# Kernel tuning notes

Measured on AMD Instinct MI355X. Metric: run time of the kernel, lower is better.

## Reference

```python
import jax, jax.numpy as jnp
import numpy as np
from jax import lax


def _conv_block(x, w, b):
    # conv5x5 stride1 VALID + bias, ReLU, maxpool 2x2 stride 2 (NCHW)
    y = lax.conv_general_dilated(x, w, (1, 1), 'VALID',
                                 dimension_numbers=('NCHW', 'OIHW', 'NCHW'))
    y = jax.nn.relu(y + b[None, :, None, None])
    return lax.reduce_window(y, -np.inf, lax.max, (1, 1, 2, 2), (1, 1, 2, 2), 'VALID')


def _attention(feat, g, w, b):
    # feat: [B,C,H,W]; g: [B,512]; Linear(512 -> C)
    q = g @ w.T + b  # [B,C]
    Bn, C, H, W = feat.shape
    f = feat.reshape(Bn, C, H * W)
    # compat_scores[b,n] = sum_c f[b,c,n] * q[b,c] ; softmax over spatial dim
    a = jax.nn.softmax(jnp.einsum('bcn,bc->bn', f, q), axis=1)
    # weighted sum over spatial locations -> [B,C]
    return jnp.einsum('bcn,bn->bc', f, a)


def setup_inputs() -> dict:
    key = jax.random.key(0)
    ks = jax.random.split(key, 12)
    s = 0.02
    f32 = jnp.float32
    return {
        'x': jax.random.normal(ks[0], (16, 1, 220, 220), f32),
        'w1': jax.random.normal(ks[1], (64, 1, 5, 5), f32) * s,
        'b1': jnp.zeros((64,), f32),
        'w2': jax.random.normal(ks[2], (128, 64, 5, 5), f32) * s,
        'b2': jnp.zeros((128,), f32),
        'w3': jax.random.normal(ks[3], (256, 128, 5, 5), f32) * s,
        'b3': jnp.zeros((256,), f32),
        'fcw': jax.random.normal(ks[4], (512, 256 * 24 * 24), f32) * 0.002,
        'fcb': jnp.zeros((512,), f32),
        'aw1': jax.random.normal(ks[5], (64, 512), f32) * s,
        'ab1': jnp.zeros((64,), f32),
        'aw2': jax.random.normal(ks[6], (128, 512), f32) * s,
        'ab2': jnp.zeros((128,), f32),
        'aw3': jax.random.normal(ks[7], (256, 512), f32) * s,
        'ab3': jnp.zeros((256,), f32),
    }


def reference(x, w1, b1, w2, b2, w3, b3, fcw, fcb, aw1, ab1, aw2, ab2, aw3, ab3):
    o1 = _conv_block(x, w1, b1)    # [B,64,108,108]
    o2 = _conv_block(o1, w2, b2)   # [B,128,52,52]
    o3 = _conv_block(o2, w3, b3)   # [B,256,24,24]
    # dropout layers are identity at inference
    flat = o3.reshape(o3.shape[0], -1)          # [B, 256*24*24]
    g = flat @ fcw.T + fcb                       # [B, 512]
    att1 = _attention(o1, g, aw1, ab1)           # [B, 64]
    att2 = _attention(o2, g, aw2, ab2)           # [B, 128]
    att3 = _attention(o3, g, aw3, ab3)           # [B, 256]
    return jnp.concatenate([att1, att2, att3], axis=1)  # [B, 448]
```

## Files before the change

### kernel.cpp

```cpp
#include <hip/hip_runtime.h>
#include <cstdint>

typedef __attribute__((ext_vector_type(8))) short short8;
typedef __attribute__((ext_vector_type(4))) float f32x4;

__device__ __forceinline__ ushort f2bf(float f) {
  union { float f; uint32_t u; } v; v.f = f;
  uint32_t u = v.u;
  return (ushort)((u + 0x7fffu + ((u >> 16) & 1u)) >> 16);
}
__device__ __forceinline__ float bf2f(ushort h) {
  union { uint32_t u; float f; } v; v.u = ((uint32_t)h) << 16;
  return v.f;
}

__global__ __launch_bounds__(256) void prelude_k(
    const float* __restrict__ x, const float* __restrict__ w1, const float* __restrict__ b1,
    const float* __restrict__ w2, const float* __restrict__ w3,
    ushort* __restrict__ o1, ushort* __restrict__ w2t, ushort* __restrict__ w3t,
    float* __restrict__ g, float* __restrict__ out) {
  __shared__ ushort sb[28 * 29];
  const int tid = threadIdx.x;
  const int bx = blockIdx.x;
  if (bx >= 1296) {
    if (bx < 4496) {
      int idx = (bx - 1296) * 256 + tid;
      if (idx < 204800) {
        int j = idx & 7, lane = (idx >> 3) & 63, ks = (idx >> 9) & 1,
            fo = (idx >> 10) & 7, kpos = idx >> 13;
        int oc = fo * 16 + (lane & 15);
        int ic = ks * 32 + (lane >> 4) * 8 + j;
        w2t[idx] = f2bf(w2[((size_t)oc * 64 + ic) * 25 + kpos]);
      }
      {
        int j = idx & 7, lane = (idx >> 3) & 63, ks = (idx >> 9) & 3,
            fo = (idx >> 11) & 15, kpos = idx >> 15;
        int oc = fo * 16 + (lane & 15);
        int ic = ks * 32 + (lane >> 4) * 8 + j;
        w3t[idx] = f2bf(w3[((size_t)oc * 128 + ic) * 25 + kpos]);
      }
    } else {
      for (int i = tid; i < 8192; i += 256) g[i] = 0.f;
      for (int i = tid; i < 7168; i += 256) out[i] = 0.f;
    }
    return;
  }
  const int b = bx / 81, rem = bx % 81, ty = rem / 9, tx = rem % 9;
  for (int i = tid; i < 784; i += 256) {
    int iy = i / 28, ix = i % 28;
    sb[iy * 29 + ix] = f2bf(x[((size_t)b * 220 + ty * 24 + iy) * 220 + tx * 24 + ix]);
  }
  __syncthreads();
  const int lane = tid & 63, wid = tid >> 6;
  const int m16 = lane & 15, qd = lane >> 4;
  short8 bfr[4];
#pragma unroll
  for (int n = 0; n < 4; n++) {
    union { ushort u[8]; short8 v; } t;
#pragma unroll
    for (int j = 0; j < 8; j++) {
      int k = qd * 8 + j;
      int kc = k < 25 ? k : 0;
      ushort val = f2bf(w1[(n * 16 + m16) * 25 + kc]);
      t.u[j] = (k < 25) ? val : (ushort)0;
    }
    bfr[n] = t.v;
  }
  int offs[8];
#pragma unroll
  for (int j = 0; j < 8; j++) {
    int k = qd * 8 + j;
    int kc = k < 25 ? k : 24;
    offs[j] = (kc / 5) * 29 + (kc % 5);
  }
  float bias[4];
#pragma unroll
  for (int n = 0; n < 4; n++) bias[n] = b1[n * 16 + m16];
  for (int gg = 0; gg < 9; gg++) {
    int gr = wid * 9 + gg;
    int wglob = gr * 4 + (m16 >> 2);
    int wy = wglob / 12, wx = wglob % 12;
    int py = wy * 2 + ((m16 >> 1) & 1), px = wx * 2 + (m16 & 1);
    int base = py * 29 + px;
    union { ushort u[8]; short8 v; } a;
#pragma unroll
    for (int j = 0; j < 8; j++) a.u[j] = sb[base + offs[j]];
    int wgd = gr * 4 + qd;
    int gy = ty * 12 + wgd / 12, gx = tx * 12 + wgd % 12;
    size_t oidx = (((size_t)b * 108 + gy) * 108 + gx) * 64;
#pragma unroll
    for (int n = 0; n < 4; n++) {
      f32x4 d = (f32x4){0.f, 0.f, 0.f, 0.f};
      d = __builtin_amdgcn_mfma_f32_16x16x32_bf16(a.v, bfr[n], d, 0, 0, 0);
      float mx = fmaxf(fmaxf(d[0], d[1]), fmaxf(d[2], d[3]));
      o1[oidx + n * 16 + m16] = f2bf(fmaxf(mx + bias[n], 0.f));
    }
  }
}

template <int IC, int ICP, int OCT, int WOC, int INW, int POOLW>
__global__ __launch_bounds__(256, 3) void conv_mfma(const ushort* __restrict__ in,
                                                    const ushort* __restrict__ wt,
                                                    const float* __restrict__ bias,
                                                    ushort* __restrict__ out) {
  constexpr int NB = 4 / WOC;
  constexpr int NPIX = 144;
  constexpr int PSTRIDE = OCT + 8;
  constexpr int LDSA = NB * NPIX * ICP;
  constexpr int LDSP = NB * 64 * PSTRIDE;
  constexpr int LDSN = (LDSA > LDSP) ? LDSA : LDSP;
  constexpr int NKS = IC / 32;
  constexpr int NFRAG = OCT / 16;
  __shared__ ushort sm[LDSN];
  const int tid = threadIdx.x;
  const int wid = tid >> 6, lane = tid & 63;
  const int m16 = lane & 15, qd = lane >> 4;
  const int bh = wid / WOC, og = wid % WOC;
  const int b0 = blockIdx.z * NB;
  const int ty = blockIdx.y, tx = blockIdx.x;
  {
    constexpr int C8 = IC / 8;
    for (int i = tid; i < NB * NPIX * C8; i += 256) {
      int bb = i / (NPIX * C8), rem = i % (NPIX * C8);
      int px = rem / C8, c8 = rem % C8;
      int gy = ty * 8 + px / 12, gx = tx * 8 + px % 12;
      uint4 v = *(const uint4*)(in + (((size_t)(b0 + bb) * INW + gy) * INW + gx) * IC + c8 * 8);
      *(uint4*)&sm[(bb * NPIX + px) * ICP + c8 * 8] = v;
    }
  }
  __syncthreads();
  f32x4 acc[4][4];
#pragma unroll
  for (int i = 0; i < 4; i++)
#pragma unroll
    for (int j = 0; j < 4; j++) acc[i][j] = (f32x4){0.f, 0.f, 0.f, 0.f};
  int aoff[4];
#pragma unroll
  for (int ms = 0; ms < 4; ms++) {
    int p = ms * 16 + m16;
    aoff[ms] = (bh * NPIX + (p >> 3) * 12 + (p & 7)) * ICP + qd * 8;
  }
  const int fo0 = og * 4;
  for (int ky = 0; ky < 5; ky++) {
#pragma unroll
    for (int kx = 0; kx < 5; kx++) {
      const int koff = (ky * 12 + kx) * ICP;
      const ushort* wkp = wt + (((size_t)(ky * 5 + kx) * NFRAG + fo0) * NKS) * 512 + lane * 8;
#pragma unroll
      for (int ks = 0; ks < NKS; ks++) {
        short8 afr[4], bfr[4];
#pragma unroll
        for (int ms = 0; ms < 4; ms++)
          afr[ms] = *(const short8*)&sm[aoff[ms] + koff + ks * 32];
#pragma unroll
        for (int ns = 0; ns < 4; ns++)
          bfr[ns] = *(const short8*)(wkp + (ns * NKS + ks) * 512);
#pragma unroll
        for (int ms = 0; ms < 4; ms++)
#pragma unroll
          for (int ns = 0; ns < 4; ns++)
            acc[ms][ns] = __builtin_amdgcn_mfma_f32_16x16x32_bf16(afr[ms], bfr[ns], acc[ms][ns], 0, 0, 0);
      }
    }
  }
  __syncthreads();
#pragma unroll
  for (int ms = 0; ms < 4; ms++)
#pragma unroll
    for (int ns = 0; ns < 4; ns++) {
      int ocl = og * 64 + ns * 16 + m16;
      float bv = bias[ocl];
#pragma unroll
      for (int r = 0; r < 4; r++) {
        int p = ms * 16 + qd * 4 + r;
        sm[(bh * 64 + p) * PSTRIDE + ocl] = f2bf(fmaxf(acc[ms][ns][r] + bv, 0.f));
      }
    }
  __syncthreads();
  constexpr int OC2 = OCT / 2;
  const int oc2 = tid % OC2, pst = tid / OC2;
  for (int pp = pst; pp < NB * 16; pp += 256 / OC2) {
    int bb = pp >> 4, pl = pp & 15;
    int ppy = pl >> 2, ppx = pl & 3;
    int p00 = (ppy * 2) * 8 + ppx * 2;
    int oc = oc2 * 2;
    int base = bb * 64 * PSTRIDE;
    uint32_t v0 = *(const uint32_t*)&sm[base + p00 * PSTRIDE + oc];
    uint32_t v1 = *(const uint32_t*)&sm[base + (p00 + 1) * PSTRIDE + oc];
    uint32_t v2 = *(const uint32_t*)&sm[base + (p00 + 8) * PSTRIDE + oc];
    uint32_t v3 = *(const uint32_t*)&sm[base + (p00 + 9) * PSTRIDE + oc];
    float a0 = fmaxf(fmaxf(bf2f(v0 & 0xffff), bf2f(v1 & 0xffff)),
                     fmaxf(bf2f(v2 & 0xffff), bf2f(v3 & 0xffff)));
    float a1 = fmaxf(fmaxf(bf2f(v0 >> 16), bf2f(v1 >> 16)),
                     fmaxf(bf2f(v2 >> 16), bf2f(v3 >> 16)));
    uint32_t packed = ((uint32_t)f2bf(a1) << 16) | (uint32_t)f2bf(a0);
    int gy = ty * 4 + ppy, gx = tx * 4 + ppx;
    *(uint32_t*)&out[(((size_t)(b0 + bb) * POOLW + gy) * POOLW + gx) * OCT + oc] = packed;
  }
}

__global__ void transpose_o3(const ushort* __restrict__ o3, ushort* __restrict__ flatT) {
  __shared__ ushort t[32][33];
  const int b = blockIdx.z;
  const int n0 = blockIdx.x * 32, c0 = blockIdx.y * 32;
  const int tid = threadIdx.x;
  {
    int cl = tid & 31, r = tid >> 5;
    for (int i = 0; i < 4; i++) {
      int nl = r + i * 8;
      t[nl][cl] = o3[((size_t)b * 576 + n0 + nl) * 256 + c0 + cl];
    }
  }
  __syncthreads();
  {
    int nl = tid & 31, r = tid >> 5;
    for (int i = 0; i < 4; i++) {
      int cl = r + i * 8;
      flatT[(size_t)b * 147456 + (c0 + cl) * 576 + n0 + nl] = t[nl][cl];
    }
  }
}

__global__ void fc_mfma(const ushort* __restrict__ flatT, const float* __restrict__ fcw,
                        float* __restrict__ g) {
  const int tid = threadIdx.x;
  const int wid = tid >> 6, lane = tid & 63;
  const int m16 = lane & 15, qd = lane >> 4;
  const int jt = blockIdx.y * 256 + wid * 64;
  const int K0 = blockIdx.x * 384;
  f32x4 acc[4];
#pragma unroll
  for (int f = 0; f < 4; f++) acc[f] = (f32x4){0.f, 0.f, 0.f, 0.f};
  const ushort* ap = flatT + (size_t)m16 * 147456 + K0 + qd * 8;
  const float* bp = fcw + (size_t)(jt + m16) * 147456 + K0 + qd * 8;
#pragma unroll 2
  for (int ks = 0; ks < 12; ks++) {
    short8 a = *(const short8*)(ap + ks * 32);
#pragma unroll
    for (int f = 0; f < 4; f++) {
      const float* bpf = bp + (size_t)f * 16 * 147456 + ks * 32;
      float4 b0 = *(const float4*)bpf;
      float4 b1 = *(const float4*)(bpf + 4);
      short8 bb;
      bb[0] = (short)f2bf(b0.x); bb[1] = (short)f2bf(b0.y);
      bb[2] = (short)f2bf(b0.z); bb[3] = (short)f2bf(b0.w);
      bb[4] = (short)f2bf(b1.x); bb[5] = (short)f2bf(b1.y);
      bb[6] = (short)f2bf(b1.z); bb[7] = (short)f2bf(b1.w);
      acc[f] = __builtin_amdgcn_mfma_f32_16x16x32_bf16(a, bb, acc[f], 0, 0, 0);
    }
  }
  const int brow = qd * 4;
#pragma unroll
  for (int f = 0; f < 4; f++)
#pragma unroll
    for (int r = 0; r < 4; r++)
      atomicAdd(&g[(brow + r) * 512 + jt + f * 16 + m16], acc[f][r]);
}

__global__ __launch_bounds__(256) void qcalc(const float* __restrict__ g,
                                             const float* __restrict__ fcb,
                                             const float* __restrict__ aw1, const float* __restrict__ ab1,
                                             const float* __restrict__ aw2, const float* __restrict__ ab2,
                                             const float* __restrict__ aw3, const float* __restrict__ ab3,
                                             float* __restrict__ q) {
  const int b = blockIdx.x, tid = threadIdx.x;
  const int cpart = blockIdx.y;
  __shared__ float gs[512];
  for (int i = tid; i < 512; i += 256) gs[i] = g[b * 512 + i] + fcb[i];
  __syncthreads();
  for (int c = cpart * 224 + tid; c < cpart * 224 + 224; c += 256) {
    const float* ar;
    float acc;
    if (c < 64)       { ar = aw1 + (size_t)c * 512;         acc = ab1[c]; }
    else if (c < 192) { ar = aw2 + (size_t)(c - 64) * 512;  acc = ab2[c - 64]; }
    else              { ar = aw3 + (size_t)(c - 192) * 512; acc = ab3[c - 192]; }
#pragma unroll 4
    for (int j = 0; j < 512; j += 4) {
      float4 a4 = *(const float4*)(ar + j);
      acc += a4.x * gs[j] + a4.y * gs[j + 1] + a4.z * gs[j + 2] + a4.w * gs[j + 3];
    }
    q[b * 448 + c] = acc;
  }
}

template <int C, int COFF>
__device__ __forceinline__ void score_head(const ushort* __restrict__ f,
                                           const float* __restrict__ q,
                                           float* __restrict__ s, int N, int nblk, int b,
                                           float* sq) {
  const int tid = threadIdx.x;
  if (tid < C) sq[tid] = q[b * 448 + COFF + tid];
  __syncthreads();
  int n = nblk * 256 + tid;
  if (n >= N) return;
  const ushort* fr = f + ((size_t)b * N + n) * C;
  float acc = 0.f;
#pragma unroll
  for (int c0 = 0; c0 < C; c0 += 8) {
    uint4 v = *(const uint4*)&fr[c0];
    uint32_t arr[4] = {v.x, v.y, v.z, v.w};
#pragma unroll
    for (int k = 0; k < 4; k++) {
      acc += bf2f(arr[k] & 0xffff) * sq[c0 + 2 * k];
      acc += bf2f(arr[k] >> 16) * sq[c0 + 2 * k + 1];
    }
  }
  s[(size_t)b * N + n] = acc;
}

__global__ void scores_all(const ushort* __restrict__ o1, const ushort* __restrict__ o2,
                           const ushort* __restrict__ o3, const float* __restrict__ q,
                           float* __restrict__ s1, float* __restrict__ s2,
                           float* __restrict__ s3) {
  __shared__ float sq[256];
  const int bx = blockIdx.x, b = blockIdx.y;
  if (bx < 46)      score_head<64, 0>(o1, q, s1, 11664, bx, b, sq);
  else if (bx < 57) score_head<128, 64>(o2, q, s2, 2704, bx - 46, b, sq);
  else              score_head<256, 192>(o3, q, s3, 576, bx - 57, b, sq);
}

__global__ void stats_all(const float* __restrict__ s1, const float* __restrict__ s2,
                          const float* __restrict__ s3, float* __restrict__ st) {
  const int b = blockIdx.x, head = blockIdx.y, tid = threadIdx.x;
  const float* s; int N; float* stp;
  if (head == 0)      { s = s1; N = 11664; stp = st; }
  else if (head == 1) { s = s2; N = 2704;  stp = st + 32; }
  else                { s = s3; N = 576;   stp = st + 64; }
  const float* sb = s + (size_t)b * N;
  __shared__ float red[4];
  float m = -1e30f;
  for (int i = tid; i < N; i += 256) m = fmaxf(m, sb[i]);
  for (int o = 32; o; o >>= 1) m = fmaxf(m, __shfl_xor(m, o));
  if ((tid & 63) == 0) red[tid >> 6] = m;
  __syncthreads();
  m = fmaxf(fmaxf(red[0], red[1]), fmaxf(red[2], red[3]));
  __syncthreads();
  float l = 0.f;
  for (int i = tid; i < N; i += 256) l += __expf(sb[i] - m);
  for (int o = 32; o; o >>= 1) l += __shfl_xor(l, o);
  if ((tid & 63) == 0) red[tid >> 6] = l;
  __syncthreads();
  if (tid == 0) { stp[b * 2] = m; stp[b * 2 + 1] = red[0] + red[1] + red[2] + red[3]; }
}

template <int C, int COFF, int CHUNK>
__device__ __forceinline__ void wsum_head(const ushort* __restrict__ f,
                                          const float* __restrict__ s,
                                          const float* __restrict__ st,
                                          float* __restrict__ out, int N, int nblk, int b,
                                          float* ws, float* os) {
  const int tid = threadIdx.x;
  const float m = st[b * 2], rl = 1.f / st[b * 2 + 1];
  const float* sb = s + (size_t)b * N;
  const ushort* fb = f + (size_t)b * N * C;
  const int n0 = nblk * CHUNK;
  int n1 = n0 + CHUNK; if (n1 > N) n1 = N;
  const int L = n1 - n0;
  for (int i = tid; i < L; i += 256) ws[i] = __expf(sb[n0 + i] - m);
  for (int i = tid; i < C; i += 256) os[i] = 0.f;
  __syncthreads();
  constexpr int C2 = C / 2;
  constexpr int S2 = 256 / C2;
  const int c2 = tid % C2, sub = tid / C2;
  float a0 = 0.f, a1 = 0.f;
  for (int i = sub; i < L; i += S2) {
    uint32_t v = *(const uint32_t*)&fb[(size_t)(n0 + i) * C + c2 * 2];
    float w = ws[i];
    a0 += w * bf2f(v & 0xffff);
    a1 += w * bf2f(v >> 16);
  }
  atomicAdd(&os[c2 * 2], a0);
  atomicAdd(&os[c2 * 2 + 1], a1);
  __syncthreads();
  for (int i = tid; i < C; i += 256) atomicAdd(&out[b * 448 + COFF + i], os[i] * rl);
}

__global__ void wsum_all(const ushort* __restrict__ o1, const ushort* __restrict__ o2,
                         const ushort* __restrict__ o3, const float* __restrict__ s1,
                         const float* __restrict__ s2, const float* __restrict__ s3,
                         const float* __restrict__ st, float* __restrict__ out) {
  __shared__ float ws[488];
  __shared__ float os[256];
  const int bx = blockIdx.x, b = blockIdx.y;
  if (bx < 24)      wsum_head<64, 0, 486>(o1, s1, st, out, 11664, bx, b, ws, os);
  else if (bx < 40) wsum_head<128, 64, 169>(o2, s2, st + 32, out, 2704, bx - 24, b, ws, os);
  else              wsum_head<256, 192, 72>(o3, s3, st + 64, out, 576, bx - 40, b, ws, os);
}

extern "C" void kernel_launch(void* const* d_in, const int* in_sizes, int n_in,
                              void* d_out, int out_size, void* d_ws, size_t ws_size,
                              hipStream_t stream) {
  const float* x   = (const float*)d_in[0];
  const float* w1  = (const float*)d_in[1];
  const float* b1  = (const float*)d_in[2];
  const float* w2  = (const float*)d_in[3];
  const float* b2  = (const float*)d_in[4];
  const float* w3  = (const float*)d_in[5];
  const float* b3  = (const float*)d_in[6];
  const float* fcw = (const float*)d_in[7];
  const float* fcb = (const float*)d_in[8];
  const float* aw1 = (const float*)d_in[9];
  const float* ab1 = (const float*)d_in[10];
  const float* aw2 = (const float*)d_in[11];
  const float* ab2 = (const float*)d_in[12];
  const float* aw3 = (const float*)d_in[13];
  const float* ab3 = (const float*)d_in[14];
  float* out = (float*)d_out;
  char* ws = (char*)d_ws;

  ushort* o1    = (ushort*)(ws + 0);
  ushort* o2    = (ushort*)(ws + 23887872);
  ushort* o3    = (ushort*)(ws + 34963456);
  ushort* flatT = (ushort*)(ws + 39682048);
  ushort* w2t   = (ushort*)(ws + 44400640);
  ushort* w3t   = (ushort*)(ws + 44810240);
  float*  g     = (float*)(ws + 46448640);
  float*  s1    = (float*)(ws + 46510080);
  float*  s2    = (float*)(ws + 47256576);
  float*  s3    = (float*)(ws + 47429632);
  float*  st    = (float*)(ws + 47466496);
  float*  q     = (float*)(ws + 47466880);

  prelude_k<<<4497, 256, 0, stream>>>(x, w1, b1, w2, w3, o1, w2t, w3t, g, out);
  conv_mfma<64, 72, 128, 2, 108, 52><<<dim3(13, 13, 8), 256, 0, stream>>>(o1, w2t, b2, o2);
  conv_mfma<128, 136, 256, 4, 52, 24><<<dim3(6, 6, 16), 256, 0, stream>>>(o2, w3t, b3, o3);
  transpose_o3<<<dim3(18, 8, 16), 256, 0, stream>>>(o3, flatT);
  fc_mfma<<<dim3(384, 2), 256, 0, stream>>>(flatT, fcw, g);
  qcalc<<<dim3(16, 2), 256, 0, stream>>>(g, fcb, aw1, ab1, aw2, ab2, aw3, ab3, q);
  scores_all<<<dim3(60, 16), 256, 0, stream>>>(o1, o2, o3, q, s1, s2, s3);
  stats_all<<<dim3(16, 3), 256, 0, stream>>>(s1, s2, s3, st);
  wsum_all<<<dim3(48, 16), 256, 0, stream>>>(o1, o2, o3, s1, s2, s3, st, out);
}
```

Before: 652.0 us.

## Switch conv MFMA to 32x32x16 tiles and fuse flat transpose into conv3

The conv kernels now use the 32x32x16 bf16 MFMA instead of 16x16x32. Each wave covers the same 64x64 output tile with four larger instructions instead of sixteen, and the weight pre-pack layout is changed to match the new fragment shape. This is meant to halve the A/B fragment loads per MAC and raise MFMA throughput. Separately, conv3 now writes the channel-major flat layout directly in its pooling epilogue, so the standalone transpose kernel and its launch are removed. The cost is scattered 2-byte stores with a 576-element stride.

```diff
diff --git a/kernel.cpp b/kernel.cpp
--- a/kernel.cpp
+++ b/kernel.cpp
@@ -3,6 +3,7 @@
 
 typedef __attribute__((ext_vector_type(8))) short short8;
 typedef __attribute__((ext_vector_type(4))) float f32x4;
+typedef __attribute__((ext_vector_type(16))) float f32x16;
 
 __device__ __forceinline__ ushort f2bf(float f) {
   union { float f; uint32_t u; } v; v.f = f;
@@ -26,17 +27,17 @@
     if (bx < 4496) {
       int idx = (bx - 1296) * 256 + tid;
       if (idx < 204800) {
-        int j = idx & 7, lane = (idx >> 3) & 63, ks = (idx >> 9) & 1,
-            fo = (idx >> 10) & 7, kpos = idx >> 13;
-        int oc = fo * 16 + (lane & 15);
-        int ic = ks * 32 + (lane >> 4) * 8 + j;
+        int j = idx & 7, lane = (idx >> 3) & 63, ks = (idx >> 9) & 3,
+            fo = (idx >> 11) & 3, kpos = idx >> 13;
+        int oc = fo * 32 + (lane & 31);
+        int ic = ks * 16 + (lane >> 5) * 8 + j;
         w2t[idx] = f2bf(w2[((size_t)oc * 64 + ic) * 25 + kpos]);
       }
       {
-        int j = idx & 7, lane = (idx >> 3) & 63, ks = (idx >> 9) & 3,
-            fo = (idx >> 11) & 15, kpos = idx >> 15;
-        int oc = fo * 16 + (lane & 15);
-        int ic = ks * 32 + (lane >> 4) * 8 + j;
+        int j = idx & 7, lane = (idx >> 3) & 63, ks = (idx >> 9) & 7,
+            fo = (idx >> 12) & 7, kpos = idx >> 15;
+        int oc = fo * 32 + (lane & 31);
+        int ic = ks * 16 + (lane >> 5) * 8 + j;
         w3t[idx] = f2bf(w3[((size_t)oc * 128 + ic) * 25 + kpos]);
       }
     } else {
@@ -98,23 +99,24 @@
   }
 }
 
-template <int IC, int ICP, int OCT, int WOC, int INW, int POOLW>
+template <int IC, int ICP, int OCT, int WOC, int INW, int POOLW, bool WRITE_FLAT>
 __global__ __launch_bounds__(256, 3) void conv_mfma(const ushort* __restrict__ in,
                                                     const ushort* __restrict__ wt,
                                                     const float* __restrict__ bias,
-                                                    ushort* __restrict__ out) {
+                                                    ushort* __restrict__ out,
+                                                    ushort* __restrict__ flatT) {
   constexpr int NB = 4 / WOC;
   constexpr int NPIX = 144;
   constexpr int PSTRIDE = OCT + 8;
   constexpr int LDSA = NB * NPIX * ICP;
   constexpr int LDSP = NB * 64 * PSTRIDE;
   constexpr int LDSN = (LDSA > LDSP) ? LDSA : LDSP;
-  constexpr int NKS = IC / 32;
-  constexpr int NFRAG = OCT / 16;
+  constexpr int NKS = IC / 16;
+  constexpr int NFRAG = OCT / 32;
   __shared__ ushort sm[LDSN];
   const int tid = threadIdx.x;
   const int wid = tid >> 6, lane = tid & 63;
-  const int m16 = lane & 15, qd = lane >> 4;
+  const int l31 = lane & 31, lh = lane >> 5;
   const int bh = wid / WOC, og = wid % WOC;
   const int b0 = blockIdx.z * NB;
   const int ty = blockIdx.y, tx = blockIdx.x;
@@ -129,18 +131,20 @@
     }
   }
   __syncthreads();
-  f32x4 acc[4][4];
-#pragma unroll
-  for (int i = 0; i < 4; i++)
-#pragma unroll
-    for (int j = 0; j < 4; j++) acc[i][j] = (f32x4){0.f, 0.f, 0.f, 0.f};
-  int aoff[4];
-#pragma unroll
-  for (int ms = 0; ms < 4; ms++) {
-    int p = ms * 16 + m16;
-    aoff[ms] = (bh * NPIX + (p >> 3) * 12 + (p & 7)) * ICP + qd * 8;
-  }
-  const int fo0 = og * 4;
+  f32x16 acc[2][2];
+#pragma unroll
+  for (int i = 0; i < 2; i++)
+#pragma unroll
+    for (int j = 0; j < 2; j++)
+#pragma unroll
+      for (int r = 0; r < 16; r++) acc[i][j][r] = 0.f;
+  int aoff[2];
+#pragma unroll
+  for (int ms = 0; ms < 2; ms++) {
+    int p = ms * 32 + l31;
+    aoff[ms] = (bh * NPIX + (p >> 3) * 12 + (p & 7)) * ICP + lh * 8;
+  }
+  const int fo0 = og * 2;
   for (int ky = 0; ky < 5; ky++) {
 #pragma unroll
     for (int kx = 0; kx < 5; kx++) {
@@ -148,31 +152,31 @@
       const ushort* wkp = wt + (((size_t)(ky * 5 + kx) * NFRAG + fo0) * NKS) * 512 + lane * 8;
 #pragma unroll
       for (int ks = 0; ks < NKS; ks++) {
-        short8 afr[4], bfr[4];
-#pragma unroll
-        for (int ms = 0; ms < 4; ms++)
-          afr[ms] = *(const short8*)&sm[aoff[ms] + koff + ks * 32];
-#pragma unroll
-        for (int ns = 0; ns < 4; ns++)
+        short8 afr[2], bfr[2];
+#pragma unroll
+        for (int ms = 0; ms < 2; ms++)
+          afr[ms] = *(const short8*)&sm[aoff[ms] + koff + ks * 16];
+#pragma unroll
+        for (int ns = 0; ns < 2; ns++)
           bfr[ns] = *(const short8*)(wkp + (ns * NKS + ks) * 512);
 #pragma unroll
-        for (int ms = 0; ms < 4; ms++)
-#pragma unroll
-          for (int ns = 0; ns < 4; ns++)
-            acc[ms][ns] = __builtin_amdgcn_mfma_f32_16x16x32_bf16(afr[ms], bfr[ns], acc[ms][ns], 0, 0, 0);
+        for (int ms = 0; ms < 2; ms++)
+#pragma unroll
+          for (int ns = 0; ns < 2; ns++)
+            acc[ms][ns] = __builtin_amdgcn_mfma_f32_32x32x16_bf16(afr[ms], bfr[ns], acc[ms][ns], 0, 0, 0);
       }
     }
   }
   __syncthreads();
 #pragma unroll
-  for (int ms = 0; ms < 4; ms++)
-#pragma unroll
-    for (int ns = 0; ns < 4; ns++) {
-      int ocl = og * 64 + ns * 16 + m16;
+  for (int ms = 0; ms < 2; ms++)
+#pragma unroll
+    for (int ns = 0; ns < 2; ns++) {
+      int ocl = og * 64 + ns * 32 + l31;
       float bv = bias[ocl];
 #pragma unroll
-      for (int r = 0; r < 4; r++) {
-        int p = ms * 16 + qd * 4 + r;
+      for (int r = 0; r < 16; r++) {
+        int p = ms * 32 + (r & 3) + 8 * (r >> 2) + 4 * lh;
         sm[(bh * 64 + p) * PSTRIDE + ocl] = f2bf(fmaxf(acc[ms][ns][r] + bv, 0.f));
       }
     }
@@ -193,30 +197,14 @@
                      fmaxf(bf2f(v2 & 0xffff), bf2f(v3 & 0xffff)));
     float a1 = fmaxf(fmaxf(bf2f(v0 >> 16), bf2f(v1 >> 16)),
                      fmaxf(bf2f(v2 >> 16), bf2f(v3 >> 16)));
-    uint32_t packed = ((uint32_t)f2bf(a1) << 16) | (uint32_t)f2bf(a0);
+    ushort lo = f2bf(a0), hi = f2bf(a1);
+    uint32_t packed = ((uint32_t)hi << 16) | (uint32_t)lo;
     int gy = ty * 4 + ppy, gx = tx * 4 + ppx;
     *(uint32_t*)&out[(((size_t)(b0 + bb) * POOLW + gy) * POOLW + gx) * OCT + oc] = packed;
-  }
-}
-
-__global__ void transpose_o3(const ushort* __restrict__ o3, ushort* __restrict__ flatT) {
-  __shared__ ushort t[32][33];
-  const int b = blockIdx.z;
-  const int n0 = blockIdx.x * 32, c0 = blockIdx.y * 32;
-  const int tid = threadIdx.x;
-  {
-    int cl = tid & 31, r = tid >> 5;
-    for (int i = 0; i < 4; i++) {
-      int nl = r + i * 8;
-      t[nl][cl] = o3[((size_t)b * 576 + n0 + nl) * 256 + c0 + cl];
-    }
-  }
-  __syncthreads();
-  {
-    int nl = tid & 31, r = tid >> 5;
-    for (int i = 0; i < 4; i++) {
-      int cl = r + i * 8;
-      flatT[(size_t)b * 147456 + (c0 + cl) * 576 + n0 + nl] = t[nl][cl];
+    if (WRITE_FLAT) {
+      size_t fb = (size_t)(b0 + bb) * 147456 + gy * 24 + gx;
+      flatT[fb + (size_t)oc * 576] = lo;
+      flatT[fb + (size_t)(oc + 1) * 576] = hi;
     }
   }
 }
@@ -422,9 +410,8 @@
   float*  q     = (float*)(ws + 47466880);
 
   prelude_k<<<4497, 256, 0, stream>>>(x, w1, b1, w2, w3, o1, w2t, w3t, g, out);
-  conv_mfma<64, 72, 128, 2, 108, 52><<<dim3(13, 13, 8), 256, 0, stream>>>(o1, w2t, b2, o2);
-  conv_mfma<128, 136, 256, 4, 52, 24><<<dim3(6, 6, 16), 256, 0, stream>>>(o2, w3t, b3, o3);
-  transpose_o3<<<dim3(18, 8, 16), 256, 0, stream>>>(o3, flatT);
+  conv_mfma<64, 72, 128, 2, 108, 52, false><<<dim3(13, 13, 8), 256, 0, stream>>>(o1, w2t, b2, o2, nullptr);
+  conv_mfma<128, 136, 256, 4, 52, 24, true><<<dim3(6, 6, 16), 256, 0, stream>>>(o2, w3t, b3, o3, flatT);
   fc_mfma<<<dim3(384, 2), 256, 0, stream>>>(flatT, fcw, g);
   qcalc<<<dim3(16, 2), 256, 0, stream>>>(g, fcb, aw1, ab1, aw2, ab2, aw3, ab3, q);
   scores_all<<<dim3(60, 16), 256, 0, stream>>>(o1, o2, o3, q, s1, s2, s3);
```

Measured after the change: 698.6 us. 1.07x slower.

## Retile conv MFMA waves to span two images and split output channels across blocks

Applied to the files above, without the earlier changes.

The conv kernel now has every wave cover both images of a batch pair and a narrower slice of output channels. For the third conv, output channels are split across blocks via the z grid dimension. Each weight fragment read from global memory is reused across two images, which halves per-wave weight loads, while LDS A-fragment reads per wave double. For conv3 the input tile now holds two images, so LDS per block grows and the occupancy hint drops to 2, which may cut latency hiding.

```diff
diff --git a/kernel.cpp b/kernel.cpp
--- a/kernel.cpp
+++ b/kernel.cpp
@@ -98,25 +98,29 @@
   }
 }
 
-template <int IC, int ICP, int OCT, int WOC, int INW, int POOLW>
-__global__ __launch_bounds__(256, 3) void conv_mfma(const ushort* __restrict__ in,
-                                                    const ushort* __restrict__ wt,
-                                                    const float* __restrict__ bias,
-                                                    ushort* __restrict__ out) {
-  constexpr int NB = 4 / WOC;
+template <int IC, int ICP, int OCT, int OCB, int INW, int POOLW, int MINW>
+__global__ __launch_bounds__(256, MINW) void conv_mfma(const ushort* __restrict__ in,
+                                                       const ushort* __restrict__ wt,
+                                                       const float* __restrict__ bias,
+                                                       ushort* __restrict__ out) {
+  constexpr int NB = 2;
+  constexpr int NS = OCB / 64;
   constexpr int NPIX = 144;
-  constexpr int PSTRIDE = OCT + 8;
+  constexpr int PSTRIDE = OCB + 8;
   constexpr int LDSA = NB * NPIX * ICP;
   constexpr int LDSP = NB * 64 * PSTRIDE;
   constexpr int LDSN = (LDSA > LDSP) ? LDSA : LDSP;
   constexpr int NKS = IC / 32;
-  constexpr int NFRAG = OCT / 16;
+  constexpr int NFRAGT = OCT / 16;
+  constexpr int OCSPLIT = OCT / OCB;
   __shared__ ushort sm[LDSN];
   const int tid = threadIdx.x;
   const int wid = tid >> 6, lane = tid & 63;
   const int m16 = lane & 15, qd = lane >> 4;
-  const int bh = wid / WOC, og = wid % WOC;
-  const int b0 = blockIdx.z * NB;
+  const int og = wid;
+  const int zz = blockIdx.z;
+  const int b0 = (zz / OCSPLIT) * NB;
+  const int ocblk = (zz % OCSPLIT) * OCB;
   const int ty = blockIdx.y, tx = blockIdx.x;
   {
     constexpr int C8 = IC / 8;
@@ -129,55 +133,67 @@
     }
   }
   __syncthreads();
-  f32x4 acc[4][4];
-#pragma unroll
-  for (int i = 0; i < 4; i++)
-#pragma unroll
-    for (int j = 0; j < 4; j++) acc[i][j] = (f32x4){0.f, 0.f, 0.f, 0.f};
-  int aoff[4];
-#pragma unroll
-  for (int ms = 0; ms < 4; ms++) {
-    int p = ms * 16 + m16;
-    aoff[ms] = (bh * NPIX + (p >> 3) * 12 + (p & 7)) * ICP + qd * 8;
-  }
-  const int fo0 = og * 4;
+  f32x4 acc[NB][4][NS];
+#pragma unroll
+  for (int bb = 0; bb < NB; bb++)
+#pragma unroll
+    for (int ms = 0; ms < 4; ms++)
+#pragma unroll
+      for (int ns = 0; ns < NS; ns++) acc[bb][ms][ns] = (f32x4){0.f, 0.f, 0.f, 0.f};
+  int aoff[NB][4];
+#pragma unroll
+  for (int bb = 0; bb < NB; bb++)
+#pragma unroll
+    for (int ms = 0; ms < 4; ms++) {
+      int p = ms * 16 + m16;
+      aoff[bb][ms] = (bb * NPIX + (p >> 3) * 12 + (p & 7)) * ICP + qd * 8;
+    }
+  const int fo0 = (ocblk >> 4) + og * NS;
   for (int ky = 0; ky < 5; ky++) {
 #pragma unroll
     for (int kx = 0; kx < 5; kx++) {
       const int koff = (ky * 12 + kx) * ICP;
-      const ushort* wkp = wt + (((size_t)(ky * 5 + kx) * NFRAG + fo0) * NKS) * 512 + lane * 8;
+      const ushort* wkp = wt + (((size_t)(ky * 5 + kx) * NFRAGT + fo0) * NKS) * 512 + lane * 8;
 #pragma unroll
       for (int ks = 0; ks < NKS; ks++) {
-        short8 afr[4], bfr[4];
-#pragma unroll
-        for (int ms = 0; ms < 4; ms++)
-          afr[ms] = *(const short8*)&sm[aoff[ms] + koff + ks * 32];
-#pragma unroll
-        for (int ns = 0; ns < 4; ns++)
+        short8 bfr[NS];
+#pragma unroll
+        for (int ns = 0; ns < NS; ns++)
           bfr[ns] = *(const short8*)(wkp + (ns * NKS + ks) * 512);
-#pragma unroll
-        for (int ms = 0; ms < 4; ms++)
-#pragma unroll
-          for (int ns = 0; ns < 4; ns++)
-            acc[ms][ns] = __builtin_amdgcn_mfma_f32_16x16x32_bf16(afr[ms], bfr[ns], acc[ms][ns], 0, 0, 0);
+        short8 afr[NB][4];
+#pragma unroll
+        for (int bb = 0; bb < NB; bb++)
+#pragma unroll
+          for (int ms = 0; ms < 4; ms++)
+            afr[bb][ms] = *(const short8*)&sm[aoff[bb][ms] + koff + ks * 32];
+#pragma unroll
+        for (int bb = 0; bb < NB; bb++)
+#pragma unroll
+          for (int ms = 0; ms < 4; ms++)
+#pragma unroll
+            for (int ns = 0; ns < NS; ns++)
+              acc[bb][ms][ns] = __builtin_amdgcn_mfma_f32_16x16x32_bf16(
+                  afr[bb][ms], bfr[ns], acc[bb][ms][ns], 0, 0, 0);
       }
     }
   }
   __syncthreads();
 #pragma unroll
-  for (int ms = 0; ms < 4; ms++)
-#pragma unroll
-    for (int ns = 0; ns < 4; ns++) {
-      int ocl = og * 64 + ns * 16 + m16;
-      float bv = bias[ocl];
-#pragma unroll
-      for (int r = 0; r < 4; r++) {
-        int p = ms * 16 + qd * 4 + r;
-        sm[(bh * 64 + p) * PSTRIDE + ocl] = f2bf(fmaxf(acc[ms][ns][r] + bv, 0.f));
+  for (int bb = 0; bb < NB; bb++)
+#pragma unroll
+    for (int ms = 0; ms < 4; ms++)
+#pragma unroll
+      for (int ns = 0; ns < NS; ns++) {
+        int ocl = og * (16 * NS) + ns * 16 + m16;
+        float bv = bias[ocblk + ocl];
+#pragma unroll
+        for (int r = 0; r < 4; r++) {
+          int p = ms * 16 + qd * 4 + r;
+          sm[(bb * 64 + p) * PSTRIDE + ocl] = f2bf(fmaxf(acc[bb][ms][ns][r] + bv, 0.f));
+        }
       }
-    }
-  __syncthreads();
-  constexpr int OC2 = OCT / 2;
+  __syncthreads();
+  constexpr int OC2 = OCB / 2;
   const int oc2 = tid % OC2, pst = tid / OC2;
   for (int pp = pst; pp < NB * 16; pp += 256 / OC2) {
     int bb = pp >> 4, pl = pp & 15;
@@ -195,7 +211,7 @@
                      fmaxf(bf2f(v2 >> 16), bf2f(v3 >> 16)));
     uint32_t packed = ((uint32_t)f2bf(a1) << 16) | (uint32_t)f2bf(a0);
     int gy = ty * 4 + ppy, gx = tx * 4 + ppx;
-    *(uint32_t*)&out[(((size_t)(b0 + bb) * POOLW + gy) * POOLW + gx) * OCT + oc] = packed;
+    *(uint32_t*)&out[(((size_t)(b0 + bb) * POOLW + gy) * POOLW + gx) * OCT + ocblk + oc] = packed;
   }
 }
 
@@ -422,8 +438,8 @@
   float*  q     = (float*)(ws + 47466880);
 
   prelude_k<<<4497, 256, 0, stream>>>(x, w1, b1, w2, w3, o1, w2t, w3t, g, out);
-  conv_mfma<64, 72, 128, 2, 108, 52><<<dim3(13, 13, 8), 256, 0, stream>>>(o1, w2t, b2, o2);
-  conv_mfma<128, 136, 256, 4, 52, 24><<<dim3(6, 6, 16), 256, 0, stream>>>(o2, w3t, b3, o3);
+  conv_mfma<64, 72, 128, 128, 108, 52, 3><<<dim3(13, 13, 8), 256, 0, stream>>>(o1, w2t, b2, o2);
+  conv_mfma<128, 136, 256, 128, 52, 24, 2><<<dim3(6, 6, 16), 256, 0, stream>>>(o2, w3t, b3, o3);
   transpose_o3<<<dim3(18, 8, 16), 256, 0, stream>>>(o3, flatT);
   fc_mfma<<<dim3(384, 2), 256, 0, stream>>>(flatT, fcw, g);
   qcalc<<<dim3(16, 2), 256, 0, stream>>>(g, fcb, aw1, ab1, aw2, ab2, aw3, ab3, q);
```

Result: no change. 663.2 us (+1.7%).
